# Optimization experiments

Measured on AMD Instinct MI355X. Metric: run time of the kernel, lower is better.

## Reference

```python
import jax, jax.numpy as jnp
import numpy as np

D_MODEL = 1024
NUM_HEADS = 16
HEAD_DIM = D_MODEL // NUM_HEADS


def setup_inputs() -> dict:
    key = jax.random.key(0)
    ks = jax.random.split(key, 9)
    s = 1.0 / np.sqrt(D_MODEL)  # torch Linear default init range scale
    def lin(k):
        kw, kb = jax.random.split(k)
        W = jax.random.uniform(kw, (D_MODEL, D_MODEL), jnp.float32, -s, s)
        b = jax.random.uniform(kb, (D_MODEL,), jnp.float32, -s, s)
        return W, b
    Wq, bq = lin(ks[0])
    Wk, bk = lin(ks[1])
    Wv, bv = lin(ks[2])
    Wo, bo = lin(ks[3])
    x = jax.random.normal(ks[4], (4, 2048, D_MODEL), jnp.float32)
    return {"x": x, "Wq": Wq, "bq": bq, "Wk": Wk, "bk": bk,
            "Wv": Wv, "bv": bv, "Wo": Wo, "bo": bo}


def reference(x, Wq, bq, Wk, bk, Wv, bv, Wo, bo):
    B, S, _ = x.shape
    H, Dh = NUM_HEADS, HEAD_DIM
    scale = Dh ** -0.5
    # projections; W stored as [in, out] so y = x @ W + b
    q = (x @ Wq + bq).reshape(B, S, H, Dh).transpose(0, 2, 1, 3)  # [B,H,S,Dh]
    k = (x @ Wk + bk).reshape(B, S, H, Dh).transpose(0, 2, 1, 3)
    v = (x @ Wv + bv).reshape(B, S, H, Dh).transpose(0, 2, 1, 3)
    scores = jnp.einsum('bhqd,bhkd->bhqk', q, k) * scale  # [B,H,S,S]
    causal = jnp.tril(jnp.ones((S, S), dtype=bool))
    scores = jnp.where(causal[None, None], scores, jnp.finfo(scores.dtype).min)
    attn = jax.nn.softmax(scores, axis=-1)
    out = jnp.einsum('bhqk,bhkd->bhqd', attn, v)  # [B,H,S,Dh]
    out = out.transpose(0, 2, 1, 3).reshape(B, S, H * Dh)
    return out @ Wo + bo
```

## Files before the change

kernel.cpp:

```cpp
#include <hip/hip_runtime.h>
#include <math.h>

#define DM 1024
#define NH 16
#define DH 64
#define BB 4
#define SS 2048
#define MROWS (BB*SS)

typedef __bf16 bf16;
typedef __bf16 bf16x8 __attribute__((ext_vector_type(8)));
typedef float floatx4 __attribute__((ext_vector_type(4)));

#if __has_builtin(__builtin_amdgcn_exp2f)
#define EXP2F __builtin_amdgcn_exp2f
#else
#define EXP2F exp2f
#endif

#define QSCALE (0.125f * 1.44269504088896f)

__device__ __forceinline__ void cp16(void* lds, const void* g) {
  __builtin_amdgcn_global_load_lds(
      (__attribute__((address_space(1))) void*)(void*)g,
      (__attribute__((address_space(3))) void*)lds,
      16, 0, 0);
}

__global__ __launch_bounds__(256) void cvt_x(
    const float* __restrict__ X, bf16* __restrict__ Y) {
  int i = (blockIdx.x * 256 + threadIdx.x) * 8;
  float4 a = *(const float4*)&X[i];
  float4 b = *(const float4*)&X[i + 4];
  bf16x8 o;
  o[0] = (bf16)a.x; o[1] = (bf16)a.y; o[2] = (bf16)a.z; o[3] = (bf16)a.w;
  o[4] = (bf16)b.x; o[5] = (bf16)b.y; o[6] = (bf16)b.z; o[7] = (bf16)b.w;
  *(bf16x8*)&Y[i] = o;
}

__global__ __launch_bounds__(1024) void wtransc(
    const float* __restrict__ W0, const float* __restrict__ W1,
    const float* __restrict__ W2, const float* __restrict__ W3,
    bf16* __restrict__ T0, bf16* __restrict__ T1,
    bf16* __restrict__ T2, bf16* __restrict__ T3) {
  __shared__ float tile[32][33];
  const float* W; bf16* T;
  int z = blockIdx.z;
  if (z == 0)      { W = W0; T = T0; }
  else if (z == 1) { W = W1; T = T1; }
  else if (z == 2) { W = W2; T = T2; }
  else             { W = W3; T = T3; }
  int tx = threadIdx.x, ty = threadIdx.y;
  tile[ty][tx] = W[(blockIdx.y * 32 + ty) * DM + blockIdx.x * 32 + tx];
  __syncthreads();
  T[(blockIdx.x * 32 + ty) * DM + blockIdx.y * 32 + tx] = (bf16)tile[tx][ty];
}

#define BK 32
#define TST 136

__global__ __launch_bounds__(256, 3) void gemm_qkv(
    const bf16* __restrict__ A, const bf16* __restrict__ WT,
    const float* __restrict__ bq, const float* __restrict__ bk,
    const float* __restrict__ bv,
    bf16* __restrict__ qb, bf16* __restrict__ kb, bf16* __restrict__ vt) {
  __shared__ __align__(16) char smem[2 * 128 * BK * 2 * 2 > 128 * TST * 2
                                         ? 2 * 128 * BK * 2 * 2
                                         : 128 * TST * 2];
  bf16* As = (bf16*)smem;
  bf16* Bs = (bf16*)smem + 2 * 128 * BK;
  bf16* Ts = (bf16*)smem;

  int tid = threadIdx.x;
  int lane = tid & 63, w = tid >> 6;
  int wm = (w >> 1) * 64;
  int wn = (w & 1) * 64;
  int m0 = blockIdx.y * 128;
  int n0 = blockIdx.x * 128;
  int which = n0 >> 10;
  int qd = lane >> 4;
  int l15 = lane & 15;

  floatx4 acc[4][4] = {};

  auto stage = [&](int pb, int k0) {
    for (int i = 0; i < 2; ++i) {
      int ci = (w * 2 + i) * 64;
      int c = ci + lane;
      int r = c >> 2, cc = (c & 3) * 8;
      cp16(&As[pb * 128 * BK + ci * 8], &A[(size_t)(m0 + r) * DM + k0 + cc]);
      cp16(&Bs[pb * 128 * BK + ci * 8], &WT[(size_t)(n0 + r) * DM + k0 + cc]);
    }
  };

  stage(0, 0);
  __syncthreads();

  for (int t = 0; t < DM / BK; ++t) {
    int pb = t & 1;
    if (t + 1 < DM / BK) stage(pb ^ 1, (t + 1) * BK);
    bf16x8 af[4], bfr[4];
    for (int mt = 0; mt < 4; ++mt)
      af[mt] = *(const bf16x8*)&As[pb * 128 * BK + (wm + mt * 16 + l15) * BK + qd * 8];
    for (int nt = 0; nt < 4; ++nt)
      bfr[nt] = *(const bf16x8*)&Bs[pb * 128 * BK + (wn + nt * 16 + l15) * BK + qd * 8];
    for (int mt = 0; mt < 4; ++mt)
      for (int nt = 0; nt < 4; ++nt)
        acc[mt][nt] = __builtin_amdgcn_mfma_f32_16x16x32_bf16(
            af[mt], bfr[nt], acc[mt][nt], 0, 0, 0);
    __syncthreads();
  }

  const float* bias = (which == 0) ? bq : (which == 1) ? bk : bv;

  if (which == 2) {
    for (int nt = 0; nt < 4; ++nt) {
      int cl = wn + nt * 16 + l15;
      float bv_ = bias[(n0 & 1023) + cl];
      for (int mt = 0; mt < 4; ++mt)
        for (int r = 0; r < 4; ++r)
          Ts[cl * TST + wm + mt * 16 + qd * 4 + r] = (bf16)(acc[mt][nt][r] + bv_);
    }
    __syncthreads();
    int chunk = tid & 15, colb = tid >> 4;
    for (int p = 0; p < 8; ++p) {
      int cl = p * 16 + colb;
      bf16x8 vv = *(const bf16x8*)&Ts[cl * TST + chunk * 8];
      *(bf16x8*)&vt[(size_t)((n0 & 1023) + cl) * MROWS + m0 + chunk * 8] = vv;
    }
  } else {
    bf16* out = (which == 0) ? qb : kb;
    float sc = (which == 0) ? QSCALE : 1.0f;
    for (int nt = 0; nt < 4; ++nt) {
      int col = (n0 & 1023) + wn + nt * 16 + l15;
      float bv_ = bias[col];
      for (int mt = 0; mt < 4; ++mt)
        for (int r = 0; r < 4; ++r) {
          int row = m0 + wm + mt * 16 + qd * 4 + r;
          out[(size_t)row * DM + col] = (bf16)((acc[mt][nt][r] + bv_) * sc);
        }
    }
  }
}

__global__ __launch_bounds__(256, 4) void gemm_out(
    const bf16* __restrict__ A, const bf16* __restrict__ WT,
    const float* __restrict__ bias, float* __restrict__ C) {
  __shared__ __align__(16) bf16 As[2][64 * BK];
  __shared__ __align__(16) bf16 Bs[2][128 * BK];
  int tid = threadIdx.x;
  int lane = tid & 63, w = tid >> 6;
  int wm = (w >> 1) * 32;
  int wn = (w & 1) * 64;
  int m0 = blockIdx.x * 64;
  int n0 = blockIdx.y * 128;
  int qd = lane >> 4;
  int l15 = lane & 15;

  floatx4 acc[2][4] = {};

  auto stage = [&](int pb, int k0) {
    {
      int ci = w * 64;
      int c = ci + lane;
      int r = c >> 2, cc = (c & 3) * 8;
      cp16(&As[pb][ci * 8], &A[(size_t)(m0 + r) * DM + k0 + cc]);
    }
    for (int i = 0; i < 2; ++i) {
      int ci = (w * 2 + i) * 64;
      int c = ci + lane;
      int r = c >> 2, cc = (c & 3) * 8;
      cp16(&Bs[pb][ci * 8], &WT[(size_t)(n0 + r) * DM + k0 + cc]);
    }
  };

  stage(0, 0);
  __syncthreads();

  for (int t = 0; t < DM / BK; ++t) {
    int pb = t & 1;
    if (t + 1 < DM / BK) stage(pb ^ 1, (t + 1) * BK);
    bf16x8 af[2], bfr[4];
    for (int mt = 0; mt < 2; ++mt)
      af[mt] = *(const bf16x8*)&As[pb][(wm + mt * 16 + l15) * BK + qd * 8];
    for (int nt = 0; nt < 4; ++nt)
      bfr[nt] = *(const bf16x8*)&Bs[pb][(wn + nt * 16 + l15) * BK + qd * 8];
    for (int mt = 0; mt < 2; ++mt)
      for (int nt = 0; nt < 4; ++nt)
        acc[mt][nt] = __builtin_amdgcn_mfma_f32_16x16x32_bf16(
            af[mt], bfr[nt], acc[mt][nt], 0, 0, 0);
    __syncthreads();
  }

  for (int nt = 0; nt < 4; ++nt) {
    int col = n0 + wn + nt * 16 + l15;
    float bv = bias[col];
    for (int mt = 0; mt < 2; ++mt)
      for (int r = 0; r < 4; ++r) {
        int row = m0 + wm + mt * 16 + qd * 4 + r;
        C[(size_t)row * DM + col] = acc[mt][nt][r] + bv;
      }
  }
}

__global__ __launch_bounds__(256, 2) void attn_fwd(
    const bf16* __restrict__ Qg, const bf16* __restrict__ Kg,
    const bf16* __restrict__ Vt, bf16* __restrict__ O) {
  __shared__ __align__(16) bf16 Kbuf[2][64 * 64];
  __shared__ __align__(16) bf16 Vbuf[2][64 * 64];
  __shared__ __align__(16) bf16 Ps[4][32][72];

  int tid = threadIdx.x;
  int lane = tid & 63, w = tid >> 6;
  int qd = lane >> 4, l15 = lane & 15;
  int sw = l15 & 7;
  int pair = blockIdx.x, h = blockIdx.y, b = blockIdx.z;
  int base = b * SS;
  int hoff = h * DH;

  int gch = ((lane & 7) ^ (lane >> 3)) * 8;
  auto stage = [&](int pb, int kt) {
    int kbase = base + kt * 64;
    for (int i = 0; i < 2; ++i) {
      int ci = (w * 2 + i) * 64;
      int row = (ci + lane) >> 3;
      cp16(&Kbuf[pb][ci * 8], &Kg[(size_t)(kbase + row) * DM + hoff + gch]);
      cp16(&Vbuf[pb][ci * 8],
           &Vt[(size_t)(hoff + row) * MROWS + base + kt * 64 + gch]);
    }
  };

  bf16x8 onesf;
  for (int j = 0; j < 8; ++j) onesf[j] = (bf16)1.0f;

  for (int ph = 0; ph < 2; ++ph) {
    int qt = ph ? (15 - pair) : pair;
    int q0 = qt * 128;
    int nkt = 2 * qt + 2;

    stage(0, 0);

    bf16x8 qf[2][2];
    for (int mt = 0; mt < 2; ++mt) {
      int qrow = base + q0 + w * 32 + mt * 16 + l15;
      for (int ks = 0; ks < 2; ++ks)
        qf[mt][ks] = *(const bf16x8*)&Qg[(size_t)qrow * DM + hoff + ks * 32 + qd * 8];
    }

    float m_r[2] = {-3e38f, -3e38f};
    floatx4 lacc[2] = {};
    floatx4 oacc[2][4] = {};

    __syncthreads();

    for (int kt = 0; kt < nkt; ++kt) {
      int pb = kt & 1;
      if (kt + 1 < nkt) stage(pb ^ 1, kt + 1);

      floatx4 s[2][4] = {};
      for (int ks = 0; ks < 2; ++ks)
        for (int nt = 0; nt < 4; ++nt) {
          bf16x8 kf = *(const bf16x8*)
              &Kbuf[pb][(nt * 16 + l15) * 64 + (((ks << 2) + qd) ^ sw) * 8];
          s[0][nt] = __builtin_amdgcn_mfma_f32_16x16x32_bf16(
              qf[0][ks], kf, s[0][nt], 0, 0, 0);
          s[1][nt] = __builtin_amdgcn_mfma_f32_16x16x32_bf16(
              qf[1][ks], kf, s[1][nt], 0, 0, 0);
        }

      if (kt >= 2 * qt) {
        for (int mt = 0; mt < 2; ++mt)
          for (int nt = 0; nt < 4; ++nt) {
            int col = kt * 64 + nt * 16 + l15;
            for (int r = 0; r < 4; ++r) {
              int row = q0 + w * 32 + mt * 16 + qd * 4 + r;
              if (col > row) s[mt][nt][r] = -3e38f;
            }
          }
      }

      for (int mt = 0; mt < 2; ++mt) {
        float t = s[mt][0][0];
        for (int nt = 0; nt < 4; ++nt)
          for (int r = 0; r < 4; ++r) t = fmaxf(t, s[mt][nt][r]);
        t = fmaxf(t, __shfl_xor(t, 1, 64));
        t = fmaxf(t, __shfl_xor(t, 2, 64));
        t = fmaxf(t, __shfl_xor(t, 4, 64));
        t = fmaxf(t, __shfl_xor(t, 8, 64));
        float mn = fmaxf(m_r[mt], t);
        float al = EXP2F(m_r[mt] - mn);
        m_r[mt] = mn;
        for (int dt = 0; dt < 4; ++dt)
          for (int r = 0; r < 4; ++r) oacc[mt][dt][r] *= al;
        for (int r = 0; r < 4; ++r) lacc[mt][r] *= al;
        for (int nt = 0; nt < 4; ++nt)
          for (int r = 0; r < 4; ++r) {
            float p = EXP2F(s[mt][nt][r] - mn);
            Ps[w][mt * 16 + qd * 4 + r][nt * 16 + l15] = (bf16)p;
          }
      }

      bf16x8 pf[2][2];
      for (int mt = 0; mt < 2; ++mt)
        for (int ks = 0; ks < 2; ++ks)
          pf[mt][ks] = *(const bf16x8*)&Ps[w][mt * 16 + l15][ks * 32 + qd * 8];

      for (int ks = 0; ks < 2; ++ks)
        for (int dt = 0; dt < 4; ++dt) {
          bf16x8 vf = *(const bf16x8*)
              &Vbuf[pb][(dt * 16 + l15) * 64 + (((ks << 2) + qd) ^ sw) * 8];
          oacc[0][dt] = __builtin_amdgcn_mfma_f32_16x16x32_bf16(
              pf[0][ks], vf, oacc[0][dt], 0, 0, 0);
          oacc[1][dt] = __builtin_amdgcn_mfma_f32_16x16x32_bf16(
              pf[1][ks], vf, oacc[1][dt], 0, 0, 0);
        }
      for (int mt = 0; mt < 2; ++mt)
        for (int ks = 0; ks < 2; ++ks)
          lacc[mt] = __builtin_amdgcn_mfma_f32_16x16x32_bf16(
              pf[mt][ks], onesf, lacc[mt], 0, 0, 0);

      __syncthreads();
    }

    for (int mt = 0; mt < 2; ++mt)
      for (int r = 0; r < 4; ++r) {
        float inv = 1.0f / lacc[mt][r];
        int row = base + q0 + w * 32 + mt * 16 + qd * 4 + r;
        for (int dt = 0; dt < 4; ++dt)
          O[(size_t)row * DM + hoff + dt * 16 + l15] = (bf16)(oacc[mt][dt][r] * inv);
      }
  }
}

extern "C" void kernel_launch(void* const* d_in, const int* in_sizes, int n_in,
                              void* d_out, int out_size, void* d_ws, size_t ws_size,
                              hipStream_t stream) {
  const float* x  = (const float*)d_in[0];
  const float* Wq = (const float*)d_in[1];
  const float* bq = (const float*)d_in[2];
  const float* Wk = (const float*)d_in[3];
  const float* bk = (const float*)d_in[4];
  const float* Wv = (const float*)d_in[5];
  const float* bv = (const float*)d_in[6];
  const float* Wo = (const float*)d_in[7];
  const float* bo = (const float*)d_in[8];
  float* out = (float*)d_out;

  char* ws = (char*)d_ws;
  const size_t act = (size_t)MROWS * DM * sizeof(bf16);
  bf16* xb    = (bf16*)(ws);
  bf16* qb    = (bf16*)(ws + act);
  bf16* kb    = (bf16*)(ws + 2 * act);
  bf16* vt    = (bf16*)(ws + 3 * act);
  bf16* ab    = (bf16*)(ws + 4 * act);
  bf16* WqkvT = (bf16*)(ws + 5 * act);
  bf16* WoT   = WqkvT + 3 * (size_t)DM * DM;

  cvt_x<<<MROWS * DM / (256 * 8), 256, 0, stream>>>(x, xb);
  wtransc<<<dim3(32, 32, 4), dim3(32, 32), 0, stream>>>(
      Wq, Wk, Wv, Wo,
      WqkvT, WqkvT + (size_t)DM * DM, WqkvT + 2 * (size_t)DM * DM, WoT);

  gemm_qkv<<<dim3(24, 64), 256, 0, stream>>>(
      xb, WqkvT, bq, bk, bv, qb, kb, vt);

  attn_fwd<<<dim3(8, NH, BB), 256, 0, stream>>>(qb, kb, vt, ab);

  gemm_out<<<dim3(128, 8), 256, 0, stream>>>(ab, WoT, bo, out);
}
```

Baseline: 272.4 us.

## Split attention work across 8 waves with 16 query rows each

```diff
diff --git a/kernel.cpp b/kernel.cpp
--- a/kernel.cpp
+++ b/kernel.cpp
@@ -203,12 +203,12 @@
   }
 }
 
-__global__ __launch_bounds__(256, 2) void attn_fwd(
+__global__ __launch_bounds__(512, 4) void attn_fwd(
     const bf16* __restrict__ Qg, const bf16* __restrict__ Kg,
     const bf16* __restrict__ Vt, bf16* __restrict__ O) {
   __shared__ __align__(16) bf16 Kbuf[2][64 * 64];
   __shared__ __align__(16) bf16 Vbuf[2][64 * 64];
-  __shared__ __align__(16) bf16 Ps[4][32][72];
+  __shared__ __align__(16) bf16 Ps[8][16][72];
 
   int tid = threadIdx.x;
   int lane = tid & 63, w = tid >> 6;
@@ -221,13 +221,11 @@
   int gch = ((lane & 7) ^ (lane >> 3)) * 8;
   auto stage = [&](int pb, int kt) {
     int kbase = base + kt * 64;
-    for (int i = 0; i < 2; ++i) {
-      int ci = (w * 2 + i) * 64;
-      int row = (ci + lane) >> 3;
-      cp16(&Kbuf[pb][ci * 8], &Kg[(size_t)(kbase + row) * DM + hoff + gch]);
-      cp16(&Vbuf[pb][ci * 8],
-           &Vt[(size_t)(hoff + row) * MROWS + base + kt * 64 + gch]);
-    }
+    int ci = w * 64;
+    int row = (ci + lane) >> 3;
+    cp16(&Kbuf[pb][ci * 8], &Kg[(size_t)(kbase + row) * DM + hoff + gch]);
+    cp16(&Vbuf[pb][ci * 8],
+         &Vt[(size_t)(hoff + row) * MROWS + base + kt * 64 + gch]);
   };
 
   bf16x8 onesf;
@@ -240,16 +238,16 @@
 
     stage(0, 0);
 
-    bf16x8 qf[2][2];
-    for (int mt = 0; mt < 2; ++mt) {
-      int qrow = base + q0 + w * 32 + mt * 16 + l15;
-      for (int ks = 0; ks < 2; ++ks)
-        qf[mt][ks] = *(const bf16x8*)&Qg[(size_t)qrow * DM + hoff + ks * 32 + qd * 8];
-    }
-
-    float m_r[2] = {-3e38f, -3e38f};
-    floatx4 lacc[2] = {};
-    floatx4 oacc[2][4] = {};
+    bf16x8 qf[2];
+    {
+      int qrow = base + q0 + w * 16 + l15;
+      for (int ks = 0; ks < 2; ++ks)
+        qf[ks] = *(const bf16x8*)&Qg[(size_t)qrow * DM + hoff + ks * 32 + qd * 8];
+    }
+
+    float m_r = -3e38f;
+    floatx4 lacc = {};
+    floatx4 oacc[4] = {};
 
     __syncthreads();
 
@@ -257,78 +255,70 @@
       int pb = kt & 1;
       if (kt + 1 < nkt) stage(pb ^ 1, kt + 1);
 
-      floatx4 s[2][4] = {};
+      floatx4 s[4] = {};
       for (int ks = 0; ks < 2; ++ks)
         for (int nt = 0; nt < 4; ++nt) {
           bf16x8 kf = *(const bf16x8*)
               &Kbuf[pb][(nt * 16 + l15) * 64 + (((ks << 2) + qd) ^ sw) * 8];
-          s[0][nt] = __builtin_amdgcn_mfma_f32_16x16x32_bf16(
-              qf[0][ks], kf, s[0][nt], 0, 0, 0);
-          s[1][nt] = __builtin_amdgcn_mfma_f32_16x16x32_bf16(
-              qf[1][ks], kf, s[1][nt], 0, 0, 0);
+          s[nt] = __builtin_amdgcn_mfma_f32_16x16x32_bf16(
+              qf[ks], kf, s[nt], 0, 0, 0);
         }
 
       if (kt >= 2 * qt) {
-        for (int mt = 0; mt < 2; ++mt)
-          for (int nt = 0; nt < 4; ++nt) {
-            int col = kt * 64 + nt * 16 + l15;
-            for (int r = 0; r < 4; ++r) {
-              int row = q0 + w * 32 + mt * 16 + qd * 4 + r;
-              if (col > row) s[mt][nt][r] = -3e38f;
-            }
+        for (int nt = 0; nt < 4; ++nt) {
+          int col = kt * 64 + nt * 16 + l15;
+          for (int r = 0; r < 4; ++r) {
+            int row = q0 + w * 16 + qd * 4 + r;
+            if (col > row) s[nt][r] = -3e38f;
           }
+        }
       }
 
-      for (int mt = 0; mt < 2; ++mt) {
-        float t = s[mt][0][0];
+      {
+        float t = s[0][0];
         for (int nt = 0; nt < 4; ++nt)
-          for (int r = 0; r < 4; ++r) t = fmaxf(t, s[mt][nt][r]);
+          for (int r = 0; r < 4; ++r) t = fmaxf(t, s[nt][r]);
         t = fmaxf(t, __shfl_xor(t, 1, 64));
         t = fmaxf(t, __shfl_xor(t, 2, 64));
         t = fmaxf(t, __shfl_xor(t, 4, 64));
         t = fmaxf(t, __shfl_xor(t, 8, 64));
-        float mn = fmaxf(m_r[mt], t);
-        float al = EXP2F(m_r[mt] - mn);
-        m_r[mt] = mn;
+        float mn = fmaxf(m_r, t);
+        float al = EXP2F(m_r - mn);
+        m_r = mn;
         for (int dt = 0; dt < 4; ++dt)
-          for (int r = 0; r < 4; ++r) oacc[mt][dt][r] *= al;
-        for (int r = 0; r < 4; ++r) lacc[mt][r] *= al;
+          for (int r = 0; r < 4; ++r) oacc[dt][r] *= al;
+        for (int r = 0; r < 4; ++r) lacc[r] *= al;
         for (int nt = 0; nt < 4; ++nt)
           for (int r = 0; r < 4; ++r) {
-            float p = EXP2F(s[mt][nt][r] - mn);
-            Ps[w][mt * 16 + qd * 4 + r][nt * 16 + l15] = (bf16)p;
+            float p = EXP2F(s[nt][r] - mn);
+            Ps[w][qd * 4 + r][nt * 16 + l15] = (bf16)p;
           }
       }
 
-      bf16x8 pf[2][2];
-      for (int mt = 0; mt < 2; ++mt)
-        for (int ks = 0; ks < 2; ++ks)
-          pf[mt][ks] = *(const bf16x8*)&Ps[w][mt * 16 + l15][ks * 32 + qd * 8];
+      bf16x8 pf[2];
+      for (int ks = 0; ks < 2; ++ks)
+        pf[ks] = *(const bf16x8*)&Ps[w][l15][ks * 32 + qd * 8];
 
       for (int ks = 0; ks < 2; ++ks)
         for (int dt = 0; dt < 4; ++dt) {
           bf16x8 vf = *(const bf16x8*)
               &Vbuf[pb][(dt * 16 + l15) * 64 + (((ks << 2) + qd) ^ sw) * 8];
-          oacc[0][dt] = __builtin_amdgcn_mfma_f32_16x16x32_bf16(
-              pf[0][ks], vf, oacc[0][dt], 0, 0, 0);
-          oacc[1][dt] = __builtin_amdgcn_mfma_f32_16x16x32_bf16(
-              pf[1][ks], vf, oacc[1][dt], 0, 0, 0);
+          oacc[dt] = __builtin_amdgcn_mfma_f32_16x16x32_bf16(
+              pf[ks], vf, oacc[dt], 0, 0, 0);
         }
-      for (int mt = 0; mt < 2; ++mt)
-        for (int ks = 0; ks < 2; ++ks)
-          lacc[mt] = __builtin_amdgcn_mfma_f32_16x16x32_bf16(
-              pf[mt][ks], onesf, lacc[mt], 0, 0, 0);
+      for (int ks = 0; ks < 2; ++ks)
+        lacc = __builtin_amdgcn_mfma_f32_16x16x32_bf16(
+            pf[ks], onesf, lacc, 0, 0, 0);
 
       __syncthreads();
     }
 
-    for (int mt = 0; mt < 2; ++mt)
-      for (int r = 0; r < 4; ++r) {
-        float inv = 1.0f / lacc[mt][r];
-        int row = base + q0 + w * 32 + mt * 16 + qd * 4 + r;
-        for (int dt = 0; dt < 4; ++dt)
-          O[(size_t)row * DM + hoff + dt * 16 + l15] = (bf16)(oacc[mt][dt][r] * inv);
-      }
+    for (int r = 0; r < 4; ++r) {
+      float inv = 1.0f / lacc[r];
+      int row = base + q0 + w * 16 + qd * 4 + r;
+      for (int dt = 0; dt < 4; ++dt)
+        O[(size_t)row * DM + hoff + dt * 16 + l15] = (bf16)(oacc[dt][r] * inv);
+    }
   }
 }
 
@@ -364,7 +354,7 @@
   gemm_qkv<<<dim3(24, 64), 256, 0, stream>>>(
       xb, WqkvT, bq, bk, bv, qb, kb, vt);
 
-  attn_fwd<<<dim3(8, NH, BB), 256, 0, stream>>>(qb, kb, vt, ab);
+  attn_fwd<<<dim3(8, NH, BB), 512, 0, stream>>>(qb, kb, vt, ab);
 
   gemm_out<<<dim3(128, 8), 256, 0, stream>>>(ab, WoT, bo, out);
 }
```

Result: no change. 268.3 us (-1.5%).
